# Kernel tuning notes

Measured on AMD Instinct MI355X. Metric: run time of the kernel, lower is better.

## Reference

```python
import jax, jax.numpy as jnp
import numpy as np
import math

B, T, E = 1, 2048, 2048
H, D = 16, 128
L = 64
RA_WINDOW = 64
RA_ALPHA = 0.5


def setup_inputs() -> dict:
    key = jax.random.key(0)
    ks = jax.random.split(key, 7)
    s_e = 1.0 / math.sqrt(E)
    s_l = 1.0 / math.sqrt(L)
    return {
        "hidden_states": jax.random.normal(ks[0], (B, T, E), jnp.float32),
        "Wq": jax.random.normal(ks[1], (E, E), jnp.float32) * s_e,       # q_proj.weight [out,in]
        "Wk": jax.random.normal(ks[2], (L, E), jnp.float32) * s_e,       # k_down.weight
        "Wv": jax.random.normal(ks[3], (L, E), jnp.float32) * s_e,       # v_down.weight
        "q_to_latent": jax.random.normal(ks[4], (H, D, L), jnp.float32) * (1.0 / math.sqrt(D)),
        "v_up": jax.random.normal(ks[5], (H, L, D), jnp.float32) * s_l,
        "Wo": jax.random.normal(ks[6], (E, E), jnp.float32) * s_e,       # out_proj.weight
    }


def reference(hidden_states, Wq, Wk, Wv, q_to_latent, v_up, Wo):
    B_, T_, E_ = hidden_states.shape
    NEG = jnp.asarray(-1e30, hidden_states.dtype)

    # per-head queries [B,T,H,D]
    Q = (hidden_states @ Wq.T).reshape(B_, T_, H, D)
    # shared latent K/V [B,T,L]
    latent_k = hidden_states @ Wk.T
    latent_v = hidden_states @ Wv.T

    # per-head Q -> latent alignment [B,T,H,L]
    q_latent = jnp.einsum('bthd,hdl->bthl', Q, q_to_latent)

    inv_sqrt_L = 1.0 / math.sqrt(L)
    # main latent-compressed logits [B,H,T,T]
    logits = jnp.einsum('bthl,bsl->bhts', q_latent, latent_k) * inv_sqrt_L

    i = jnp.arange(T_)[:, None]
    j = jnp.arange(T_)[None, :]
    causal = j <= i                       # [T,T]
    logits = jnp.where(causal[None, None], logits, NEG)

    # reciprocal band pass. NOTE: einsum labels (d vs l) intentionally mismatch,
    # faithfully reproducing the source's outer-product-of-sums computation.
    logits_recip = jnp.einsum('bthd,bsl->bhts', q_latent, latent_k) * inv_sqrt_L
    band = (jnp.abs(i - j) <= RA_WINDOW) & causal
    logits = jnp.where(band[None, None], logits + RA_ALPHA * logits_recip, logits)

    attn = jax.nn.softmax(logits, axis=-1)  # [B,H,T,T]

    # per-head V up-projection [B,T,H,D]
    V_exp = jnp.einsum('btl,hld->bthd', latent_v, v_up)
    ctx = jnp.einsum('bhts,bshd->bthd', attn, V_exp)
    out = ctx.reshape(B_, T_, H * D) @ Wo.T
    return out
```

## Files before the change

### kernel.cpp

```cpp
#include <hip/hip_runtime.h>


#define T_ 2048
#define E_ 2048
#define H_ 16
#define D_ 128
#define L_ 64
#define NQ 1152

typedef float  floatx4 __attribute__((ext_vector_type(4)));
typedef __bf16 bf16x8  __attribute__((ext_vector_type(8)));

__device__ __forceinline__ ushort f2b(float x){
  unsigned int u = __float_as_uint(x);
  u = (u + 0x7fffu + ((u >> 16) & 1u)) >> 16;
  return (ushort)u;
}
__device__ __forceinline__ float blo(unsigned int u){ return __uint_as_float(u << 16); }
__device__ __forceinline__ float bhi(unsigned int u){ return __uint_as_float(u & 0xffff0000u); }

__device__ __forceinline__ void glds16(const ushort* g, ushort* l){
#if __has_builtin(__builtin_amdgcn_global_load_lds)
  __builtin_amdgcn_global_load_lds((const __attribute__((address_space(1))) void*)g,
                                   (__attribute__((address_space(3))) void*)l, 16, 0, 0);
#else
  *(uint4*)l = *(const uint4*)g;
#endif
}

__global__ __launch_bounds__(256)
void k_f2b4(const float* __restrict__ a, ushort* __restrict__ oa,
            const float* __restrict__ b, ushort* __restrict__ ob,
            const float* __restrict__ c, ushort* __restrict__ oc,
            const float* __restrict__ d, ushort* __restrict__ od){
  int bid = blockIdx.x; const float* src; ushort* dst; int base;
  if (bid < 4096){ src=a; dst=oa; base=bid; }
  else if (bid < 8192){ src=b; dst=ob; base=bid-4096; }
  else if (bid < 8320){ src=c; dst=oc; base=bid-8192; }
  else { src=d; dst=od; base=bid-8320; }
  int i = (base*256 + (int)threadIdx.x)*4;
  float4 v = *(const float4*)(src + i);
  ushort4 o; o.x=f2b(v.x); o.y=f2b(v.y); o.z=f2b(v.z); o.w=f2b(v.w);
  *(ushort4*)(dst + i) = o;
}

__global__ __launch_bounds__(128)
void k_prep_wql(const float* __restrict__ Wq, const float* __restrict__ q2l,
                ushort* __restrict__ Wql){
  const int h = blockIdx.z, lh = blockIdx.y;
  const int e = blockIdx.x*128 + threadIdx.x;
  const float* qb = q2l + (size_t)h*D_*L_ + lh*32;
  float acc[32];
  #pragma unroll
  for (int i=0;i<32;++i) acc[i]=0.f;
  for (int d=0; d<128; ++d){
    float wv = Wq[(size_t)(h*128+d)*E_ + e];
    #pragma unroll
    for (int i=0;i<32;++i) acc[i] += wv*qb[(size_t)d*64 + i];
  }
  #pragma unroll
  for (int i=0;i<32;++i) Wql[(size_t)(h*64 + lh*32 + i)*E_ + e] = f2b(acc[i]);
}

__global__ __launch_bounds__(256)
void k_prep_vupT(const float* __restrict__ vup, ushort* __restrict__ vupT){
  const int h = blockIdx.x, tid = threadIdx.x;
  for (int idx = tid; idx < L_*D_; idx += 256){
    int l = idx >> 7, d = idx & 127;
    vupT[(size_t)h*D_*L_ + d*64 + l] = f2b(vup[(size_t)h*L_*D_ + idx]);
  }
}

template<int MT,int NT,bool OB16>
__global__ __launch_bounds__(256)
void gemm_glds(const ushort* __restrict__ A, const ushort* __restrict__ B,
               float* __restrict__ Cf, ushort* __restrict__ Cb,
               int M, int N, int K, float scale){
  constexpr int BM = 32*MT, BN = 32*NT;
  constexpr int IA = BM/64, IB = BN/64;
  __shared__ ushort As[BM*32];
  __shared__ ushort Bs[BN*32];
  const int tid = threadIdx.x, lane = tid&63, wv = tid>>6;
  const int wm = wv & 1, wn = wv >> 1;
  const int l15 = lane&15, quad = lane>>4;
  const int m0 = blockIdx.y*BM, n0 = blockIdx.x*BN;
  const float sc = (n0 < 1024) ? scale : 1.0f;
  floatx4 acc[MT][NT] = {};
  for (int k0=0; k0<K; k0+=32){
    __syncthreads();
    #pragma unroll
    for (int j=0;j<IA;++j){
      int c = (j*4 + wv)*64 + lane; int row = c>>2, kc = (c&3)*8;
      glds16(A + (size_t)(m0+row)*K + k0 + kc, &As[c*8]);
    }
    #pragma unroll
    for (int j=0;j<IB;++j){
      int c = (j*4 + wv)*64 + lane; int row = c>>2, kc = (c&3)*8;
      glds16(B + (size_t)(n0+row)*K + k0 + kc, &Bs[c*8]);
    }
    __syncthreads();
    bf16x8 af[MT], bfr[NT];
    #pragma unroll
    for (int mi=0;mi<MT;++mi)
      af[mi] = *(const bf16x8*)(&As[(wm*MT*16 + mi*16 + l15)*32 + quad*8]);
    #pragma unroll
    for (int ni=0;ni<NT;++ni)
      bfr[ni] = *(const bf16x8*)(&Bs[(wn*NT*16 + ni*16 + l15)*32 + quad*8]);
    #pragma unroll
    for (int mi=0;mi<MT;++mi)
      #pragma unroll
      for (int ni=0;ni<NT;++ni)
        acc[mi][ni] = __builtin_amdgcn_mfma_f32_16x16x32_bf16(af[mi], bfr[ni], acc[mi][ni], 0,0,0);
  }
  #pragma unroll
  for (int mi=0;mi<MT;++mi){
    const int rb = m0 + wm*MT*16 + mi*16 + quad*4;
    #pragma unroll
    for (int ni=0;ni<NT;++ni){
      const int col = n0 + wn*NT*16 + ni*16 + l15;
      #pragma unroll
      for (int r=0;r<4;++r){
        if constexpr (OB16) Cb[(size_t)(rb+r)*N + col] = f2b(acc[mi][ni][r]*sc);
        else                Cf[(size_t)(rb+r)*N + col] = acc[mi][ni][r];
      }
    }
  }
}

__global__ __launch_bounds__(256)
void k_rowsums(const ushort* __restrict__ qkvb,
               float* __restrict__ rsq, float* __restrict__ rsk){
  int i = blockIdx.x*256 + threadIdx.x;
  const ushort* src; float* dst;
  if (i < T_*H_){
    int t = i>>4, g = i&15;
    src = qkvb + (size_t)t*NQ + g*64; dst = rsq + i;
  } else {
    int t = i - T_*H_;
    if (t >= T_) return;
    src = qkvb + (size_t)t*NQ + 1024; dst = rsk + t;
  }
  const uint4* p = (const uint4*)src;
  float s = 0.f;
  #pragma unroll
  for (int j=0;j<8;++j){
    uint4 u = p[j];
    const unsigned int uu[4] = {u.x,u.y,u.z,u.w};
    #pragma unroll
    for (int q=0;q<4;++q){ s += blo(uu[q]); s += bhi(uu[q]); }
  }
  *dst = s;
}

__global__ __launch_bounds__(256)
void k_vexp_mfma(const ushort* __restrict__ qkvb, const ushort* __restrict__ vupT,
                 ushort* __restrict__ vexpT){
  const int h = blockIdx.y, t0 = blockIdx.x*64;
  const int tid = threadIdx.x, lane = tid&63, w = tid>>6;
  const int l15 = lane&15, quad = lane>>4;
  bf16x8 a[2][2], b[4][2];
  #pragma unroll
  for (int mt=0;mt<2;++mt)
    #pragma unroll
    for (int kk=0;kk<2;++kk)
      a[mt][kk] = *(const bf16x8*)(vupT + (size_t)h*D_*L_ + (w*32+mt*16+l15)*64 + kk*32 + quad*8);
  #pragma unroll
  for (int nt=0;nt<4;++nt)
    #pragma unroll
    for (int kk=0;kk<2;++kk)
      b[nt][kk] = *(const bf16x8*)(qkvb + (size_t)(t0+nt*16+l15)*NQ + 1088 + kk*32 + quad*8);
  floatx4 acc[2][4] = {};
  #pragma unroll
  for (int mt=0;mt<2;++mt)
    #pragma unroll
    for (int nt=0;nt<4;++nt)
      #pragma unroll
      for (int kk=0;kk<2;++kk)
        acc[mt][nt] = __builtin_amdgcn_mfma_f32_16x16x32_bf16(a[mt][kk], b[nt][kk], acc[mt][nt], 0,0,0);
  #pragma unroll
  for (int mt=0;mt<2;++mt)
    #pragma unroll
    for (int nt=0;nt<4;++nt)
      #pragma unroll
      for (int r=0;r<4;++r)
        vexpT[((size_t)h*D_ + w*32+mt*16+quad*4+r)*T_ + t0 + nt*16 + l15] = f2b(acc[mt][nt][r]);
}

__global__ __launch_bounds__(256, 4)
void k_attn(const ushort* __restrict__ qkvb,
            const float*  __restrict__ rsq,
            const float*  __restrict__ rsk,
            const ushort* __restrict__ vexpT,
            ushort*       __restrict__ ctx,
            ushort*       __restrict__ partO,
            float*        __restrict__ partML,
            int CH){
  __shared__ ushort Ks[64*64];
  __shared__ ushort Vts[128*64];
  __shared__ ushort Ps[4*16*64];
  const int h  = blockIdx.y;
  const int bxr = (int)gridDim.x - 1 - (int)blockIdx.x;
  int qt, c;
  if (CH == 8){
    if (bxr < 8){ qt = bxr; c = 0; }
    else if (bxr < 24){ int u = bxr-8;  qt = 8  + (u>>1); c = u&1; }
    else if (bxr < 48){ int u = bxr-24; qt = 16 + u/3;    c = u - (u/3)*3; }
    else               { int u = bxr-48; qt = 24 + (u>>2); c = u&3; }
  } else { qt = bxr; c = 0; }
  const int nct = (qt + CH) / CH;
  const int stBeg = c*CH, stEnd = min(qt, stBeg + CH - 1);
  const int t0 = qt*64;
  const int tid = threadIdx.x, lane = tid & 63, w = tid >> 6;
  const int l15 = lane & 15, quad = lane >> 4;

  auto stageK = [&](int s0k){
    #pragma unroll
    for (int j=0;j<2;++j){ int cc = tid + j*256;
      int row = cc>>3, kc = ((cc&7) ^ (row&7))*8;
      glds16(qkvb + (size_t)(s0k + row)*NQ + 1024 + kc, &Ks[cc*8]); }
  };
  auto stageV = [&](int s0v){
    #pragma unroll
    for (int j=0;j<4;++j){ int cc = tid + j*256;
      int row = cc>>3, sc2 = ((cc&7) ^ (row&7))*8;
      glds16(vexpT + ((size_t)h*128 + row)*T_ + s0v + sc2, &Vts[cc*8]); }
  };

  const int qrow = t0 + w*16 + l15;
  const bf16x8 q0 = *(const bf16x8*)(qkvb + (size_t)qrow*NQ + h*64 + quad*8);
  const bf16x8 q1 = *(const bf16x8*)(qkvb + (size_t)qrow*NQ + h*64 + 32 + quad*8);
  const float rqv = rsq[(size_t)qrow*H_ + h] * 0.5f;

  float mrun = -INFINITY, lrun = 0.f;
  floatx4 o[8] = {};

  stageK(stBeg*64); stageV(stBeg*64);

  for (int st=stBeg; st<=stEnd; ++st){
    const int s0 = st*64;
    const bool more = (st < stEnd);
    asm volatile("s_waitcnt vmcnt(4)" ::: "memory");
    __builtin_amdgcn_s_barrier();
    __builtin_amdgcn_sched_barrier(0);
    floatx4 sT[4] = {};
    __builtin_amdgcn_s_setprio(1);
    #pragma unroll
    for (int jt=0;jt<4;++jt){
      const int srow = jt*16 + l15, sx = srow & 7;
      bf16x8 k0f = *(const bf16x8*)(&Ks[srow*64 + (quad^sx)*8]);
      sT[jt] = __builtin_amdgcn_mfma_f32_16x16x32_bf16(k0f, q0, sT[jt], 0,0,0);
      bf16x8 k1f = *(const bf16x8*)(&Ks[srow*64 + ((4+quad)^sx)*8]);
      sT[jt] = __builtin_amdgcn_mfma_f32_16x16x32_bf16(k1f, q1, sT[jt], 0,0,0);
    }
    __builtin_amdgcn_s_setprio(0);
    __builtin_amdgcn_sched_barrier(0);
    __builtin_amdgcn_s_barrier();
    if (more) stageK(s0 + 64);
    float mloc = -3.0e38f;
    if (st >= qt-1){
      #pragma unroll
      for (int jt=0;jt<4;++jt){
        const float4 rk4 = *(const float4*)(rsk + s0 + jt*16 + quad*4);
        #pragma unroll
        for (int r=0;r<4;++r){
          const int sg = s0 + jt*16 + quad*4 + r;
          const int dd = qrow - sg;
          float x = sT[jt][r];
          x = (dd <= 64) ? x + rqv*((const float*)&rk4)[r] : x;
          x = (dd < 0)   ? -3.0e38f : x;
          sT[jt][r] = x; mloc = fmaxf(mloc, x);
        }
      }
    } else {
      #pragma unroll
      for (int jt=0;jt<4;++jt)
        #pragma unroll
        for (int r=0;r<4;++r) mloc = fmaxf(mloc, sT[jt][r]);
    }
    mloc = fmaxf(mloc, __shfl_xor(mloc, 16));
    mloc = fmaxf(mloc, __shfl_xor(mloc, 32));
    const float mn = (mloc - mrun <= 6.0f) ? mrun : mloc;
    const float al = exp2f(mrun - mn);
    float ss = 0.f;
    #pragma unroll
    for (int jt=0;jt<4;++jt)
      #pragma unroll
      for (int r=0;r<4;++r){
        float p = exp2f(sT[jt][r]-mn); sT[jt][r] = p; ss += p;
      }
    ss += __shfl_xor(ss, 16); ss += __shfl_xor(ss, 32);
    lrun = lrun*al + ss; mrun = mn;
    #pragma unroll
    for (int jt=0;jt<4;++jt){
      unsigned p01, p23;
      asm volatile("v_cvt_pk_bf16_f32 %0, %1, %2" : "=v"(p01) : "v"(sT[jt][0]), "v"(sT[jt][1]));
      asm volatile("v_cvt_pk_bf16_f32 %0, %1, %2" : "=v"(p23) : "v"(sT[jt][2]), "v"(sT[jt][3]));
      const int chunk = 2*jt + (quad>>1);
      uint2 pw2; pw2.x = p01; pw2.y = p23;
      *(uint2*)(&Ps[(w*16 + l15)*64 + ((chunk ^ (l15&7))<<3) + (quad&1)*4]) = pw2;
    }
    if (__any(al < 1.0f)){
      float alr[4];
      #pragma unroll
      for (int r=0;r<4;++r) alr[r] = __shfl(al, quad*4 + r);
      #pragma unroll
      for (int nt=0;nt<8;++nt){
        o[nt][0]*=alr[0]; o[nt][1]*=alr[1]; o[nt][2]*=alr[2]; o[nt][3]*=alr[3];
      }
    }
    __builtin_amdgcn_sched_barrier(0);
    if (more) asm volatile("s_waitcnt vmcnt(2)" ::: "memory");
    else      asm volatile("s_waitcnt vmcnt(0)" ::: "memory");
    __builtin_amdgcn_s_barrier();
    __builtin_amdgcn_sched_barrier(0);
    __builtin_amdgcn_s_setprio(1);
    #pragma unroll
    for (int kks=0;kks<2;++kks){
      const int ch = kks*4 + quad;
      bf16x8 pf = *(const bf16x8*)(&Ps[(w*16 + l15)*64 + ((ch ^ (l15&7))<<3)]);
      #pragma unroll
      for (int nt=0;nt<8;++nt){
        const int vrow = nt*16 + l15, vx = vrow & 7;
        bf16x8 vf = *(const bf16x8*)(&Vts[vrow*64 + ((kks*4+quad)^vx)*8]);
        o[nt] = __builtin_amdgcn_mfma_f32_16x16x32_bf16(pf, vf, o[nt], 0,0,0);
      }
    }
    __builtin_amdgcn_s_setprio(0);
    __builtin_amdgcn_sched_barrier(0);
    if (more){
      __builtin_amdgcn_s_barrier();
      stageV(s0 + 64);
    }
  }
  const float linv = 1.f/lrun;
  float lr4[4];
  #pragma unroll
  for (int r=0;r<4;++r) lr4[r] = __shfl(linv, quad*4 + r);
  if (nct == 1){
    #pragma unroll
    for (int r=0;r<4;++r){
      const int row = t0 + w*16 + quad*4 + r;
      #pragma unroll
      for (int nt=0;nt<8;++nt)
        ctx[(size_t)row*E_ + h*D_ + nt*16 + l15] = f2b(o[nt][r]*lr4[r]);
    }
  } else {
    const int slot = (h*24 + (qt-8))*4 + c;
    ushort* po = partO + (size_t)slot*8192;
    #pragma unroll
    for (int nt=0;nt<8;++nt)
      #pragma unroll
      for (int r=0;r<4;++r)
        po[((w*8+nt)*4+r)*64 + quad*16 + l15] = f2b(o[nt][r]*lr4[r]);
    if (quad == 0){
      float2 ml; ml.x = mrun; ml.y = lrun;
      ((float2*)partML)[(size_t)slot*64 + w*16 + l15] = ml;
    }
  }
}

__global__ __launch_bounds__(256)
void k_merge(const ushort* __restrict__ partO, const float* __restrict__ partML,
             ushort* __restrict__ ctx){
  const int h = blockIdx.y, qt = 8 + blockIdx.x;
  const int nct = (qt + 8) / 8;
  const int tid = threadIdx.x;
  const int rg = tid >> 2, d0 = (tid & 3)*32;
  const int w = rg >> 4, quad = (rg >> 2) & 3, rr = rg & 3;
  const int n0 = d0 >> 4;
  const int sbase = (h*24 + (qt-8))*4;
  float m[4], l[4], M = -INFINITY;
  for (int c=0;c<4;++c){
    if (c < nct){
      float2 v = ((const float2*)partML)[(size_t)(sbase+c)*64 + rg];
      m[c]=v.x; l[c]=v.y; M = fmaxf(M, v.x);
    }
  }
  float lt = 0.f, wgt[4];
  for (int c=0;c<4;++c){
    if (c < nct){ wgt[c] = exp2f(m[c]-M)*l[c]; lt += wgt[c]; }
  }
  const float inv = 1.f/lt;
  float acc[32];
  #pragma unroll
  for (int i=0;i<32;++i) acc[i]=0.f;
  for (int c=0;c<4;++c){
    if (c >= nct) break;
    const float sc = wgt[c]*inv;
    const ushort* po = partO + (size_t)(sbase+c)*8192;
    #pragma unroll
    for (int nn=0;nn<2;++nn){
      const ushort* p2 = po + ((w*8 + n0+nn)*4 + rr)*64 + quad*16;
      uint4 u  = *(const uint4*)p2;
      uint4 u2 = *(const uint4*)(p2 + 8);
      const unsigned int uu[8] = {u.x,u.y,u.z,u.w,u2.x,u2.y,u2.z,u2.w};
      #pragma unroll
      for (int q=0;q<8;++q){
        acc[nn*16+q*2]   += sc*blo(uu[q]);
        acc[nn*16+q*2+1] += sc*bhi(uu[q]);
      }
    }
  }
  ushort* dst = ctx + (size_t)(qt*64 + rg)*E_ + h*D_ + d0;
  #pragma unroll
  for (int k=0;k<8;++k){
    ushort4 ov; ov.x=f2b(acc[k*4]); ov.y=f2b(acc[k*4+1]);
    ov.z=f2b(acc[k*4+2]); ov.w=f2b(acc[k*4+3]);
    *(ushort4*)(dst + k*4) = ov;
  }
}

extern "C" void kernel_launch(void* const* d_in, const int* in_sizes, int n_in,
                              void* d_out, int out_size, void* d_ws, size_t ws_size,
                              hipStream_t stream) {
  const float* hs  = (const float*)d_in[0];
  const float* Wq  = (const float*)d_in[1];
  const float* Wk  = (const float*)d_in[2];
  const float* Wv  = (const float*)d_in[3];
  const float* q2l = (const float*)d_in[4];
  const float* vup = (const float*)d_in[5];
  const float* Wo  = (const float*)d_in[6];
  float* out = (float*)d_out;
  char* ws = (char*)d_ws;

  ushort* hsb   = (ushort*)(ws + 0);
  ushort* Wqkvb = (ushort*)(ws + 8388608);
  ushort* Wob   = (ushort*)(ws + 13107200);
  ushort* qkvb  = (ushort*)(ws + 21495808);
  ushort* vupT  = (ushort*)(ws + 26214400);
  float*  rsqp  = (float*) (ws + 26476544);
  float*  rskp  = (float*) (ws + 26607616);
  ushort* vexpT = (ushort*)(ws + 26615808);
  ushort* ctxb  = (ushort*)(ws + 35004416);
  ushort* partO = (ushort*)(ws + 43393024);
  float*  partML= (float*) (ws + 68558848);
  const size_t NEED = 69345280;
  const int CH = (ws_size >= NEED) ? 8 : 32;

  k_f2b4<<<8448, 256, 0, stream>>>(hs, hsb, Wo, Wob,
                                   Wk, Wqkvb + (size_t)1024*E_,
                                   Wv, Wqkvb + (size_t)1088*E_);

  k_prep_wql<<<dim3(16,2,16), 128, 0, stream>>>(Wq, q2l, Wqkvb);
  k_prep_vupT<<<16, 256, 0, stream>>>(vup, vupT);

  gemm_glds<2,2,true><<<dim3(18,32), 256, 0, stream>>>(
      hsb, Wqkvb, nullptr, qkvb, T_, NQ, E_, 0.18033688f);

  k_rowsums<<<136, 256, 0, stream>>>(qkvb, rsqp, rskp);

  k_vexp_mfma<<<dim3(32,16), 256, 0, stream>>>(qkvb, vupT, vexpT);

  k_attn<<<dim3(CH==8 ? 80 : 32, 16), 256, 0, stream>>>(
      qkvb, rsqp, rskp, vexpT, ctxb, partO, partML, CH);

  if (CH == 8)
    k_merge<<<dim3(24,16), 256, 0, stream>>>(partO, partML, ctxb);

  gemm_glds<2,4,false><<<dim3(16,32), 256, 0, stream>>>(
      ctxb, Wob, out, nullptr, T_, E_, E_, 1.0f);
}
```

Before: 272.2 us.

## Double GEMM K-tile to 64 with XOR-swizzled LDS and XCD-aware block remap

The bf16 MFMA GEMM now stages 64-wide K slices per iteration instead of 32, halving the number of barrier/load rounds. The LDS layout uses an XOR swizzle on 16-byte chunks to avoid bank conflicts on fragment reads. Block IDs are remapped so that consecutive tiles are spread across the 8 XCDs. The cost is doubled LDS per block, which may reduce occupancy.

```diff
diff --git a/kernel.cpp b/kernel.cpp
--- a/kernel.cpp
+++ b/kernel.cpp
@@ -73,44 +73,54 @@
 
 template<int MT,int NT,bool OB16>
 __global__ __launch_bounds__(256)
-void gemm_glds(const ushort* __restrict__ A, const ushort* __restrict__ B,
-               float* __restrict__ Cf, ushort* __restrict__ Cb,
-               int M, int N, int K, float scale){
+void gemm_glds2(const ushort* __restrict__ A, const ushort* __restrict__ B,
+                float* __restrict__ Cf, ushort* __restrict__ Cb,
+                int M, int N, int K, float scale){
   constexpr int BM = 32*MT, BN = 32*NT;
-  constexpr int IA = BM/64, IB = BN/64;
-  __shared__ ushort As[BM*32];
-  __shared__ ushort Bs[BN*32];
+  constexpr int IA = BM/32, IB = BN/32;
+  __shared__ ushort As[BM*64];
+  __shared__ ushort Bs[BN*64];
   const int tid = threadIdx.x, lane = tid&63, wv = tid>>6;
   const int wm = wv & 1, wn = wv >> 1;
   const int l15 = lane&15, quad = lane>>4;
-  const int m0 = blockIdx.y*BM, n0 = blockIdx.x*BN;
+  const int nbx = (int)gridDim.x, nwg = nbx*(int)gridDim.y;
+  int bid = (int)blockIdx.y*nbx + (int)blockIdx.x;
+  bid = (bid & 7)*(nwg >> 3) + (bid >> 3);
+  const int m0 = (bid / nbx)*BM, n0 = (bid % nbx)*BN;
   const float sc = (n0 < 1024) ? scale : 1.0f;
   floatx4 acc[MT][NT] = {};
-  for (int k0=0; k0<K; k0+=32){
+  for (int k0=0; k0<K; k0+=64){
     __syncthreads();
     #pragma unroll
     for (int j=0;j<IA;++j){
-      int c = (j*4 + wv)*64 + lane; int row = c>>2, kc = (c&3)*8;
-      glds16(A + (size_t)(m0+row)*K + k0 + kc, &As[c*8]);
+      int cc = j*256 + tid; int row = cc>>3, kc = ((cc&7)^(row&7))*8;
+      glds16(A + (size_t)(m0+row)*K + k0 + kc, &As[cc*8]);
     }
     #pragma unroll
     for (int j=0;j<IB;++j){
-      int c = (j*4 + wv)*64 + lane; int row = c>>2, kc = (c&3)*8;
-      glds16(B + (size_t)(n0+row)*K + k0 + kc, &Bs[c*8]);
+      int cc = j*256 + tid; int row = cc>>3, kc = ((cc&7)^(row&7))*8;
+      glds16(B + (size_t)(n0+row)*K + k0 + kc, &Bs[cc*8]);
     }
     __syncthreads();
-    bf16x8 af[MT], bfr[NT];
-    #pragma unroll
-    for (int mi=0;mi<MT;++mi)
-      af[mi] = *(const bf16x8*)(&As[(wm*MT*16 + mi*16 + l15)*32 + quad*8]);
-    #pragma unroll
-    for (int ni=0;ni<NT;++ni)
-      bfr[ni] = *(const bf16x8*)(&Bs[(wn*NT*16 + ni*16 + l15)*32 + quad*8]);
-    #pragma unroll
-    for (int mi=0;mi<MT;++mi)
-      #pragma unroll
-      for (int ni=0;ni<NT;++ni)
-        acc[mi][ni] = __builtin_amdgcn_mfma_f32_16x16x32_bf16(af[mi], bfr[ni], acc[mi][ni], 0,0,0);
+    #pragma unroll
+    for (int kk=0;kk<2;++kk){
+      bf16x8 af[MT], bfr[NT];
+      #pragma unroll
+      for (int mi=0;mi<MT;++mi){
+        const int r = wm*MT*16 + mi*16 + l15;
+        af[mi] = *(const bf16x8*)(&As[r*64 + (((kk*4+quad)^(r&7))<<3)]);
+      }
+      #pragma unroll
+      for (int ni=0;ni<NT;++ni){
+        const int r = wn*NT*16 + ni*16 + l15;
+        bfr[ni] = *(const bf16x8*)(&Bs[r*64 + (((kk*4+quad)^(r&7))<<3)]);
+      }
+      #pragma unroll
+      for (int mi=0;mi<MT;++mi)
+        #pragma unroll
+        for (int ni=0;ni<NT;++ni)
+          acc[mi][ni] = __builtin_amdgcn_mfma_f32_16x16x32_bf16(af[mi], bfr[ni], acc[mi][ni], 0,0,0);
+    }
   }
   #pragma unroll
   for (int mi=0;mi<MT;++mi){
@@ -444,7 +454,7 @@
   k_prep_wql<<<dim3(16,2,16), 128, 0, stream>>>(Wq, q2l, Wqkvb);
   k_prep_vupT<<<16, 256, 0, stream>>>(vup, vupT);
 
-  gemm_glds<2,2,true><<<dim3(18,32), 256, 0, stream>>>(
+  gemm_glds2<2,2,true><<<dim3(18,32), 256, 0, stream>>>(
       hsb, Wqkvb, nullptr, qkvb, T_, NQ, E_, 0.18033688f);
 
   k_rowsums<<<136, 256, 0, stream>>>(qkvb, rsqp, rskp);
@@ -457,6 +467,6 @@
   if (CH == 8)
     k_merge<<<dim3(24,16), 256, 0, stream>>>(partO, partML, ctxb);
 
-  gemm_glds<2,4,false><<<dim3(16,32), 256, 0, stream>>>(
+  gemm_glds2<2,4,false><<<dim3(16,32), 256, 0, stream>>>(
       ctxb, Wob, out, nullptr, T_, E_, E_, 1.0f);
 }
```

Result: faster. 254.5 us (-6.5%).
